# Performance work log

Hardware: AMD Instinct MI355X
Metric: run time of the kernel (lower is better)

The kernel has to match this reference:

```python
import jax, jax.numpy as jnp
import numpy as np

G = 16       # groups
GRID = 25    # hardcoded self.grid
EPS = 1e-5   # BatchNorm eps


def _gconv(x, w, pad):
    # x: (B, Cin, H, W), w: (Cout, Cin//G, kh, kw); grouped conv, stride 1
    return jax.lax.conv_general_dilated(
        x, w, window_strides=(1, 1), padding=[(pad, pad), (pad, pad)],
        feature_group_count=G)


def _bn_relu(h, g, b, m, v):
    # h: (G, B, C, H, W); per-group-instance BN params: (G, C). Inference BN.
    scale = (g / jnp.sqrt(v + EPS))[:, None, :, None, None]
    return jax.nn.relu((h - m[:, None, :, None, None]) * scale + b[:, None, :, None, None])


def setup_inputs() -> dict:
    key = jax.random.key(0)
    ks = jax.random.split(key, 11)
    B, C, H, W = 2, 256, 24, 24
    AC = GRID * C  # 6400 affinity channels
    return {
        "x":  jax.random.normal(ks[0], (B, C, H, W), jnp.float32),
        "W1": jax.random.normal(ks[1], (G, C, C // G, 3, 3), jnp.float32) * 0.05,
        "g1": jax.random.uniform(ks[2], (G, C), jnp.float32, 0.5, 1.5),
        "b1": jax.random.normal(ks[3], (G, C), jnp.float32) * 0.1,
        "m1": jax.random.normal(ks[4], (G, C), jnp.float32) * 0.1,
        "v1": jax.random.uniform(ks[5], (G, C), jnp.float32, 0.5, 1.5),
        "W2": jax.random.normal(ks[6], (G, AC, C // G, 1, 1), jnp.float32) * 0.05,
        "g2": jax.random.uniform(ks[7], (G, AC), jnp.float32, 0.5, 1.5),
        "b2": jax.random.normal(ks[8], (G, AC), jnp.float32) * 0.1,
        "m2": jax.random.normal(ks[9], (G, AC), jnp.float32) * 0.1,
        "v2": jax.random.uniform(ks[10], (G, AC), jnp.float32, 0.5, 1.5),
    }


def reference(x, W1, g1, b1, m1, v1, W2, g2, b2, m2, v2):
    B, C, H, W = x.shape
    Cg = C // G
    # 16 independent grouped 3x3 convs over the same input, batched via vmap
    h1 = jax.vmap(lambda w: _gconv(x, w, 1))(W1)          # (G, B, C, H, W)
    h1 = _bn_relu(h1, g1, b1, m1, v1)
    # grouped 1x1 conv with padding=1 (faithful to source -> spatial grows to H+2, W+2)
    a = jax.vmap(lambda h, w: _gconv(h, w, 1))(h1, W2)    # (G, B, 25C, H+2, W+2)
    a = _bn_relu(a, g2, b2, m2, v2)
    pooled = a.mean(axis=(-2, -1))                        # adaptive avg pool -> (G, B, 25C)
    xv = pooled.reshape(G, B, G, GRID * Cg)               # (G, B, G, 25*Cg)
    aff = jnp.einsum('ibkm,iblm->ibkl', xv, xv)           # (G, B, G, G) = theta @ phi
    idx = jnp.arange(G)
    aff_i = aff[idx, :, idx, :] / G                       # aff[:, i], /N  -> (G, B, G)
    ex = h1.reshape(G, B, G, Cg * H * W)
    # torch.matmul((B,G), (B,G,M)) broadcasts 2-D lhs -> (B, B, M); kept faithfully
    z = jnp.einsum('ipk,iqkm->ipqm', aff_i, ex)           # (G, B, B, Cg*H*W)
    z = z.reshape(G, B, B, Cg, H, W).transpose(1, 0, 2, 3, 4, 5)
    return z.reshape(B, G * B * Cg, H, W)                 # (B, B*C, H, W)
```

## Files before the change

### kernel.cpp

```cpp
#include <hip/hip_runtime.h>
#include <hip/hip_bf16.h>


typedef __attribute__((ext_vector_type(8))) short short8;
typedef __attribute__((ext_vector_type(4))) float f32x4;

static __device__ __forceinline__ unsigned short f2bf(float x) {
    unsigned u = __float_as_uint(x);
    unsigned r = (u + 0x7fffu + ((u >> 16) & 1u)) >> 16;
    return (unsigned short)r;
}

#define WA_OFF   33696
#define WLB_OFF  23040
#define B2_OFF   35840
#define PACC_OFF 37440
#define ZP_OFF   39040
#define BB1_OFF  40096
#define SMEM_BYTES 40160

__global__ __launch_bounds__(512, 4) void k12_fused(
    const float* __restrict__ xin,
    const float* __restrict__ W1,
    const float* __restrict__ g1, const float* __restrict__ b1,
    const float* __restrict__ m1, const float* __restrict__ v1,
    const float* __restrict__ W2,
    const float* __restrict__ g2, const float* __restrict__ b2,
    const float* __restrict__ m2, const float* __restrict__ v2,
    unsigned short* __restrict__ h1b,
    float* __restrict__ pooled)
{
    __shared__ __align__(16) char smem[SMEM_BYTES];
    short* xs    = (short*)smem;
    short* wAp   = (short*)(smem + WA_OFF);
    short* hsb   = (short*)smem;
    short* wlb   = (short*)(smem + WLB_OFF);
    float* bias2 = (float*)(smem + B2_OFF);
    float* pacc  = (float*)(smem + PACC_OFF);
    float* bias1 = (float*)(smem + BB1_OFF);

    int bid = blockIdx.x;
    int i = bid >> 5, b = (bid >> 4) & 1, g = bid & 15;
    int t = threadIdx.x;

    float4 w2r[4];
    float  bsc;
    {
        bool act = (t < 400);
        int o = i*6400 + g*400 + (act ? t : 0);
        float s2 = g2[o] * rsqrtf(v2[o] + 1e-5f);
        bsc = b2[o] - m2[o] * s2;
        const float4* wr = (const float4*)&W2[o*16];
#pragma unroll
        for (int q = 0; q < 4; q++) {
            float4 wv = wr[q];
            wv.x *= s2; wv.y *= s2; wv.z *= s2; wv.w *= s2;
            w2r[q] = wv;
        }
    }

    if (t < 16) {
        int c = i*256 + g*16 + t;
        float sc = g1[c] * rsqrtf(v1[c] + 1e-5f);
        bias1[t] = b1[c] - m1[c] * sc;
    }
    {
        int* xz = (int*)xs;
        for (int idx = t; idx < 1512; idx += 512) {
            int c = idx / 12, j = idx - (idx / 12) * 12;
            int row, col;
            if (c < 26)      { row = 0;  col = c; }
            else if (c < 52) { row = 25; col = c - 26; }
            else if (c < 78) { row = 26; col = c - 52; }
            else { int k = c - 78; row = 1 + (k >> 1); col = (k & 1) ? 25 : 0; }
            xz[(row*26 + col)*12 + j] = 0;
        }
    }
    {
        const float4* xb4 = (const float4*)&xin[(b*256 + g*16)*576];
        for (int idx = t; idx < 2304; idx += 512) {
            float4 v = xb4[idx];
            int f = idx * 4;
            int ci = f / 576; int s = f - ci*576;
            int y = s / 24; int x = s - y*24;
            int base = ((y+1)*26 + (x+1))*24 + ci;
            xs[base     ] = (short)f2bf(v.x);
            xs[base + 24] = (short)f2bf(v.y);
            xs[base + 48] = (short)f2bf(v.z);
            xs[base + 72] = (short)f2bf(v.w);
        }
    }
    {
        const float* wb = &W1[(i*256 + g*16)*144];
        for (int idx = t; idx < 2560; idx += 512) {
            int kk = idx >> 9, rem = idx & 511, co = rem >> 5, k = rem & 31;
            int tap = 2*kk + (k >> 4), ci = k & 15;
            int c = i*256 + g*16 + co;
            float sc = g1[c] * rsqrtf(v1[c] + 1e-5f);
            float val = (tap < 9) ? wb[co*144 + ci*9 + tap] * sc : 0.f;
            wAp[(kk*16 + co)*40 + k] = (short)f2bf(val);
        }
    }
    __syncthreads();

    int l = t & 63, w = t >> 6;
    int quad = l >> 4, rc = l & 15;
    bool five = (w < 4);

    f32x4 dreg[5];
    {
        int ci0 = (quad & 1) * 8;
        short8 afr[5];
#pragma unroll
        for (int kk = 0; kk < 5; kk++)
            afr[kk] = *(const short8*)&wAp[(kk*16 + rc)*40 + quad*8];
        f32x4 cb1 = *(const f32x4*)&bias1[quad*4];

        const int offE[5] = {0, 48, 648, 1248, 1296};
        const int offO[5] = {24, 624, 672, 1272, 1872};
        int off[5];
#pragma unroll
        for (int kk = 0; kk < 5; kk++) off[kk] = (quad >= 2) ? offO[kk] : offE[kk];

#pragma unroll
        for (int tt = 0; tt < 5; tt++) {
            if (tt == 4 && !five) break;
            int s = (tt*8 + w)*16 + rc;
            int y = s / 24; int x = s - y*24;
            int base = (y*26 + x)*24 + ci0;
            f32x4 acc = cb1;
#pragma unroll
            for (int kk = 0; kk < 5; kk++) {
                short8 bf = *(const short8*)&xs[base + off[kk]];
                acc = __builtin_amdgcn_mfma_f32_16x16x32_bf16(afr[kk], bf, acc, 0, 0, 0);
            }
#pragma unroll
            for (int r = 0; r < 4; r++) acc[r] = fmaxf(acc[r], 0.f);
            dreg[tt] = acc;
        }
    }
    __syncthreads();

    {
        unsigned short* hout = &h1b[((i*2 + b)*256 + g*16)*576];
#pragma unroll
        for (int tt = 0; tt < 5; tt++) {
            if (tt == 4 && !five) break;
            int s = (tt*8 + w)*16 + rc;
            f32x4 acc = dreg[tt];
            unsigned short e0 = f2bf(acc[0]), e1 = f2bf(acc[1]);
            unsigned short e2 = f2bf(acc[2]), e3 = f2bf(acc[3]);
            uint2 pk = {(unsigned)e0 | ((unsigned)e1 << 16),
                        (unsigned)e2 | ((unsigned)e3 << 16)};
            *(uint2*)&hsb[s*20 + quad*4] = pk;
            hout[(quad*4 + 0)*576 + s] = e0;
            hout[(quad*4 + 1)*576 + s] = e1;
            hout[(quad*4 + 2)*576 + s] = e2;
            hout[(quad*4 + 3)*576 + s] = e3;
        }
    }
    if (t < 400) {
        pacc[t]  = 0.f;
        bias2[t] = bsc;
#pragma unroll
        for (int q = 0; q < 4; q++) {
            float4 wv = w2r[q];
            wlb[t*16 + q*4 + 0] = (short)f2bf(wv.x);
            wlb[t*16 + q*4 + 1] = (short)f2bf(wv.y);
            wlb[t*16 + q*4 + 2] = (short)f2bf(wv.z);
            wlb[t*16 + q*4 + 3] = (short)f2bf(wv.w);
        }
    }
    if (t < 4) ((int*)(smem + ZP_OFF))[t] = 0;
    __syncthreads();

    {
        int q8 = (quad & 1) * 8;
        short8 af2[5];
#pragma unroll
        for (int u = 0; u < 5; u++) {
            bool valid = (l < 32) && (u < 4 || five);
            int boff = valid ? ((((u*8 + w)*16 + rc)*20 + q8)*2) : ZP_OFF;
            af2[u] = *(const short8*)(smem + boff);
        }
        for (int mt = 0; mt < 25; mt++) {
            int m0 = mt*16;
            int woff = (l < 32) ? (WLB_OFF + ((m0 + rc)*16 + q8)*2) : ZP_OFF;
            short8 wf = *(const short8*)(smem + woff);
            float be = bias2[m0 + rc];
            f32x4 cb = {be, be, be, be};

            f32x4 accv = {0.f, 0.f, 0.f, 0.f};
#pragma unroll
            for (int u = 0; u < 4; u++) {
                f32x4 d = __builtin_amdgcn_mfma_f32_16x16x32_bf16(af2[u], wf, cb, 0, 0, 0);
#pragma unroll
                for (int r = 0; r < 4; r++)
                    accv[r] += fmaxf(d[r], 0.f);
            }
            if (five) {
                f32x4 d = __builtin_amdgcn_mfma_f32_16x16x32_bf16(af2[4], wf, cb, 0, 0, 0);
#pragma unroll
                for (int r = 0; r < 4; r++)
                    accv[r] += fmaxf(d[r], 0.f);
            }
            float a = (accv[0] + accv[1]) + (accv[2] + accv[3]);
            a += __shfl_xor(a, 16);
            a += __shfl_xor(a, 32);
            if (l < 16)
                atomicAdd(&pacc[m0 + l], a);
        }
    }
    __syncthreads();

    const float inv = 1.f / 676.f;
    if (t < 400) {
        float be = bias2[t];
        pooled[(i*2+b)*6400 + g*400 + t] =
            (pacc[t] + 100.f * fmaxf(be, 0.f)) * inv;
    }
}

__global__ __launch_bounds__(256) void k4_out(const unsigned short* __restrict__ h1b,
                                              const float* __restrict__ pooled,
                                              float* __restrict__ out)
{
    __shared__ float a0[16], a1[16];
    int bid = blockIdx.x;
    int i = bid >> 5, q = (bid >> 4) & 1, cg = bid & 15;
    int t = threadIdx.x;

    {
        int p = t >> 3, j = t & 7;
        int bb = p >> 4, l = p & 15;
        const float* pb = &pooled[(i*2 + bb)*6400];
        const float2* pth = (const float2*)(pb + i*400);
        const float2* pl  = (const float2*)(pb + l*400);
        float s = 0.f;
#pragma unroll 5
        for (int f = j; f < 200; f += 8) {
            float2 a = pth[f], c = pl[f];
            s = fmaf(a.x, c.x, s);
            s = fmaf(a.y, c.y, s);
        }
        s += __shfl_xor(s, 1);
        s += __shfl_xor(s, 2);
        s += __shfl_xor(s, 4);
        if (j == 0) {
            float v = s * (1.f/16.f);
            if (bb == 0) a0[l] = v; else a1[l] = v;
        }
    }
    __syncthreads();

    if (t >= 144) return;
    const unsigned short* hb = &h1b[((i*2+q)*256 + cg)*576];
    int ch = i*32 + q*16 + cg;
    int s = t*4;
    float c00=0.f,c01=0.f,c02=0.f,c03=0.f;
    float c10=0.f,c11=0.f,c12=0.f,c13=0.f;
#pragma unroll
    for (int k = 0; k < 16; k++) {
        uint2 hv = *(const uint2*)&hb[k*9216 + s];
        float p0 = __uint_as_float(hv.x << 16);
        float p1 = __uint_as_float(hv.x & 0xffff0000u);
        float p2 = __uint_as_float(hv.y << 16);
        float p3 = __uint_as_float(hv.y & 0xffff0000u);
        float va = a0[k], vb = a1[k];
        c00 = fmaf(va, p0, c00); c01 = fmaf(va, p1, c01);
        c02 = fmaf(va, p2, c02); c03 = fmaf(va, p3, c03);
        c10 = fmaf(vb, p0, c10); c11 = fmaf(vb, p1, c11);
        c12 = fmaf(vb, p2, c12); c13 = fmaf(vb, p3, c13);
    }
    float4 o0 = {c00, c01, c02, c03};
    float4 o1 = {c10, c11, c12, c13};
    *(float4*)&out[ch*576 + s]         = o0;
    *(float4*)&out[(512 + ch)*576 + s] = o1;
}

extern "C" void kernel_launch(void* const* d_in, const int* in_sizes, int n_in,
                              void* d_out, int out_size, void* d_ws, size_t ws_size,
                              hipStream_t stream)
{
    const float* x  = (const float*)d_in[0];
    const float* W1 = (const float*)d_in[1];
    const float* g1 = (const float*)d_in[2];
    const float* b1 = (const float*)d_in[3];
    const float* m1 = (const float*)d_in[4];
    const float* v1 = (const float*)d_in[5];
    const float* W2 = (const float*)d_in[6];
    const float* g2 = (const float*)d_in[7];
    const float* b2 = (const float*)d_in[8];
    const float* m2 = (const float*)d_in[9];
    const float* v2 = (const float*)d_in[10];

    unsigned short* h1b = (unsigned short*)d_ws;
    float* pooled = (float*)(h1b + 16*2*256*576);

    float* out = (float*)d_out;

    hipLaunchKernelGGL(k12_fused, dim3(512), dim3(512), 0, stream,
                       x, W1, g1, b1, m1, v1, W2, g2, b2, m2, v2, h1b, pooled);
    hipLaunchKernelGGL(k4_out,    dim3(512), dim3(256), 0, stream,
                       h1b, pooled, out);
}
```

Measured before the change: 111.7 us.

## Feed conv1 MFMA outputs directly as conv2 operands via 16x16x16 MFMA

The second 1x1 conv now uses the 16x16x16 bf16 MFMA so that conv1's accumulator registers can serve directly as the A operand, instead of going through a shared-memory staging buffer padded with zeros. This removes the h1 LDS write/read round trip and one of the block-wide barriers. The W2 bf16 staging is moved earlier, with packed 128-bit stores, into a separate LDS region. In exchange, LDS use per block grows from about 40 KB to about 56 KB, which may limit occupancy at 4 blocks per CU.

```diff
diff --git a/kernel.cpp b/kernel.cpp
--- a/kernel.cpp
+++ b/kernel.cpp
@@ -3,6 +3,7 @@
 
 
 typedef __attribute__((ext_vector_type(8))) short short8;
+typedef __attribute__((ext_vector_type(4))) short short4b;
 typedef __attribute__((ext_vector_type(4))) float f32x4;
 
 static __device__ __forceinline__ unsigned short f2bf(float x) {
@@ -12,12 +13,11 @@
 }
 
 #define WA_OFF   33696
-#define WLB_OFF  23040
-#define B2_OFF   35840
-#define PACC_OFF 37440
-#define ZP_OFF   39040
-#define BB1_OFF  40096
-#define SMEM_BYTES 40160
+#define WLB_OFF  40096
+#define B2_OFF   52896
+#define PACC_OFF 54496
+#define BB1_OFF  56096
+#define SMEM_BYTES 56160
 
 __global__ __launch_bounds__(512, 4) void k12_fused(
     const float* __restrict__ xin,
@@ -33,7 +33,6 @@
     __shared__ __align__(16) char smem[SMEM_BYTES];
     short* xs    = (short*)smem;
     short* wAp   = (short*)(smem + WA_OFF);
-    short* hsb   = (short*)smem;
     short* wlb   = (short*)(smem + WLB_OFF);
     float* bias2 = (float*)(smem + B2_OFF);
     float* pacc  = (float*)(smem + PACC_OFF);
@@ -101,6 +100,21 @@
             wAp[(kk*16 + co)*40 + k] = (short)f2bf(val);
         }
     }
+    if (t < 400) {
+        pacc[t]  = 0.f;
+        bias2[t] = bsc;
+        uint4 pkA, pkB;
+        pkA.x = (unsigned)f2bf(w2r[0].x) | ((unsigned)f2bf(w2r[0].y) << 16);
+        pkA.y = (unsigned)f2bf(w2r[0].z) | ((unsigned)f2bf(w2r[0].w) << 16);
+        pkA.z = (unsigned)f2bf(w2r[1].x) | ((unsigned)f2bf(w2r[1].y) << 16);
+        pkA.w = (unsigned)f2bf(w2r[1].z) | ((unsigned)f2bf(w2r[1].w) << 16);
+        pkB.x = (unsigned)f2bf(w2r[2].x) | ((unsigned)f2bf(w2r[2].y) << 16);
+        pkB.y = (unsigned)f2bf(w2r[2].z) | ((unsigned)f2bf(w2r[2].w) << 16);
+        pkB.z = (unsigned)f2bf(w2r[3].x) | ((unsigned)f2bf(w2r[3].y) << 16);
+        pkB.w = (unsigned)f2bf(w2r[3].z) | ((unsigned)f2bf(w2r[3].w) << 16);
+        *(uint4*)&wlb[t*16]     = pkA;
+        *(uint4*)&wlb[t*16 + 8] = pkB;
+    }
     __syncthreads();
 
     int l = t & 63, w = t >> 6;
@@ -139,8 +153,8 @@
             dreg[tt] = acc;
         }
     }
-    __syncthreads();
-
+
+    short4b pa[5];
     {
         unsigned short* hout = &h1b[((i*2 + b)*256 + g*16)*576];
 #pragma unroll
@@ -150,56 +164,34 @@
             f32x4 acc = dreg[tt];
             unsigned short e0 = f2bf(acc[0]), e1 = f2bf(acc[1]);
             unsigned short e2 = f2bf(acc[2]), e3 = f2bf(acc[3]);
-            uint2 pk = {(unsigned)e0 | ((unsigned)e1 << 16),
-                        (unsigned)e2 | ((unsigned)e3 << 16)};
-            *(uint2*)&hsb[s*20 + quad*4] = pk;
+            short4b pv;
+            pv[0] = (short)e0; pv[1] = (short)e1;
+            pv[2] = (short)e2; pv[3] = (short)e3;
+            pa[tt] = pv;
             hout[(quad*4 + 0)*576 + s] = e0;
             hout[(quad*4 + 1)*576 + s] = e1;
             hout[(quad*4 + 2)*576 + s] = e2;
             hout[(quad*4 + 3)*576 + s] = e3;
         }
     }
-    if (t < 400) {
-        pacc[t]  = 0.f;
-        bias2[t] = bsc;
-#pragma unroll
-        for (int q = 0; q < 4; q++) {
-            float4 wv = w2r[q];
-            wlb[t*16 + q*4 + 0] = (short)f2bf(wv.x);
-            wlb[t*16 + q*4 + 1] = (short)f2bf(wv.y);
-            wlb[t*16 + q*4 + 2] = (short)f2bf(wv.z);
-            wlb[t*16 + q*4 + 3] = (short)f2bf(wv.w);
-        }
-    }
-    if (t < 4) ((int*)(smem + ZP_OFF))[t] = 0;
-    __syncthreads();
-
-    {
-        int q8 = (quad & 1) * 8;
-        short8 af2[5];
-#pragma unroll
-        for (int u = 0; u < 5; u++) {
-            bool valid = (l < 32) && (u < 4 || five);
-            int boff = valid ? ((((u*8 + w)*16 + rc)*20 + q8)*2) : ZP_OFF;
-            af2[u] = *(const short8*)(smem + boff);
-        }
+
+    {
         for (int mt = 0; mt < 25; mt++) {
             int m0 = mt*16;
-            int woff = (l < 32) ? (WLB_OFF + ((m0 + rc)*16 + q8)*2) : ZP_OFF;
-            short8 wf = *(const short8*)(smem + woff);
+            short4b wf = *(const short4b*)&wlb[(m0 + rc)*16 + quad*4];
             float be = bias2[m0 + rc];
             f32x4 cb = {be, be, be, be};
 
             f32x4 accv = {0.f, 0.f, 0.f, 0.f};
 #pragma unroll
             for (int u = 0; u < 4; u++) {
-                f32x4 d = __builtin_amdgcn_mfma_f32_16x16x32_bf16(af2[u], wf, cb, 0, 0, 0);
+                f32x4 d = __builtin_amdgcn_mfma_f32_16x16x16bf16_1k(pa[u], wf, cb, 0, 0, 0);
 #pragma unroll
                 for (int r = 0; r < 4; r++)
                     accv[r] += fmaxf(d[r], 0.f);
             }
             if (five) {
-                f32x4 d = __builtin_amdgcn_mfma_f32_16x16x32_bf16(af2[4], wf, cb, 0, 0, 0);
+                f32x4 d = __builtin_amdgcn_mfma_f32_16x16x16bf16_1k(pa[4], wf, cb, 0, 0, 0);
 #pragma unroll
                 for (int r = 0; r < 4; r++)
                     accv[r] += fmaxf(d[r], 0.f);
```

After: 109.7 us. No clear change (-1.8%).
